# Performance work log

Hardware: AMD Instinct MI355X
Metric: run time of the kernel (lower is better)

## Reference

```python
import jax, jax.numpy as jnp
import numpy as np

NUM_EXPERTS = 8
PHM_DIM = 4


def setup_inputs() -> dict:
    key = jax.random.key(0)
    k1, k2, k3, k4 = jax.random.split(key, 4)
    bsz, seq, D, O, E, p = 4, 2048, 2048, 2048, NUM_EXPERTS, PHM_DIM
    hidden_states = jax.random.normal(k1, (bsz, seq, D), dtype=jnp.float32)
    gate_w = jax.random.normal(k2, (D, E), dtype=jnp.float32) * 0.02
    phm_rule = jax.random.normal(k3, (E, p, p, p), dtype=jnp.float32) * 0.1
    W = jax.random.normal(k4, (E, p, D // p, O // p), dtype=jnp.float32) * 0.02
    b = jnp.zeros((E, O), dtype=jnp.float32)
    return {"hidden_states": hidden_states, "gate_w": gate_w,
            "phm_rule": phm_rule, "W": W, "b": b}


def reference(hidden_states, gate_w, phm_rule, W, b):
    bsz, seq, dim = hidden_states.shape
    E = gate_w.shape[1]
    x = hidden_states.reshape(-1, dim)                      # [T, D]
    logits = x @ gate_w                                     # [T, E]
    prob = jax.nn.softmax(logits, axis=-1)                  # [T, E]
    gate = jnp.argmax(prob, axis=-1)                        # [T]
    # load-balancing loss
    num_tokens = jnp.sum(jax.nn.one_hot(gate, E, dtype=jnp.int32), axis=0)  # [E]
    f = num_tokens.astype(prob.dtype)
    f = f / jnp.sum(f)
    P = jnp.mean(prob, axis=0)
    balance_loss = E * jnp.sum(P * f)
    # PHM weight per expert: H_e = sum_p kron(phm_rule[e,p], W[e,p]) -> [E, D, O]
    Wfull = jnp.einsum('epab,epij->eaibj', phm_rule, W).reshape(E, dim, -1)
    # dense evaluation of every expert on every token, then top-1 select
    all_out = jnp.einsum('td,edo->teo', x, Wfull) + b[None, :, :]  # [T, E, O]
    tok_prob = jnp.take_along_axis(prob, gate[:, None], axis=1)    # [T, 1]
    out = jnp.take_along_axis(all_out, gate[:, None, None], axis=1)[:, 0, :] * tok_prob
    out = out.reshape(bsz, seq, -1)
    return out, balance_loss, num_tokens
```

## Files before the change

### kernel.cpp

```cpp
#include <hip/hip_runtime.h>
#include <cstdint>
#include <cstddef>

typedef _Float16 f16;
typedef f16 f16x2 __attribute__((ext_vector_type(2)));
typedef f16 f16x4 __attribute__((ext_vector_type(4)));
typedef f16 f16x8 __attribute__((ext_vector_type(8)));
typedef float f32x4 __attribute__((ext_vector_type(4)));

#define NEXP 8
#define BM 128
#define BN 128
#define BK 32
#define NSTAGE 3
#define TPW 4

__device__ __forceinline__ void async_cp16(void* lds, const void* gsrc) {
  __builtin_amdgcn_global_load_lds(
      (const __attribute__((address_space(1))) void*)gsrc,
      (__attribute__((address_space(3))) void*)lds, 16, 0, 0);
}

__global__ __launch_bounds__(256) void k_fusedA(
    const float* __restrict__ x, const float* __restrict__ gw,
    f16* __restrict__ xb, int* __restrict__ gate, float* __restrict__ scale,
    int* __restrict__ cnt, float* __restrict__ probsum,
    const float* __restrict__ Wp, const float* __restrict__ rule,
    f16* __restrict__ wt,
    int D, int Dp, int Op, int O, int ngate)
{
  __shared__ __align__(16) uint8_t smem[16960];
  int tid = threadIdx.x;

  if ((int)blockIdx.x < ngate) {
    float (*gws)[516] = (float(*)[516])smem;
    float* ps = (float*)(smem + NEXP * 516 * 4);
    int*   pc = (int*)(smem + NEXP * 516 * 4 + 32);
    int lane = tid & 63, w = tid >> 6;
    if (tid < NEXP) { ps[tid] = 0.f; pc[tid] = 0; }

    int t0 = (blockIdx.x * 4 + w) * TPW;
    const float* xr = x + (size_t)t0 * D;
    f16* xbr = xb + (size_t)t0 * D;

    float acc[TPW][NEXP] = {};
    int nq = D >> 9;
    for (int qp = 0; qp < nq; qp++) {
      __syncthreads();
      const float2* gsrc = (const float2*)(gw + (size_t)qp * 512 * NEXP);
      for (int i = tid; i < 2048; i += 256) {
        float2 v = gsrc[i];
        int f = i * 2;
        int d = f >> 3, e = f & 7;
        gws[e][d] = v.x;
        gws[e + 1][d] = v.y;
      }
      __syncthreads();

      int dh = qp << 9;
#pragma unroll
      for (int it = 0; it < 2; it++) {
        int d0 = lane * 4 + it * 256;
        float4 xv[TPW];
#pragma unroll
        for (int tp = 0; tp < TPW; tp++) {
          xv[tp] = *(const float4*)(xr + (size_t)tp * D + dh + d0);
          f16x4 h;
          h[0] = (f16)xv[tp].x; h[1] = (f16)xv[tp].y;
          h[2] = (f16)xv[tp].z; h[3] = (f16)xv[tp].w;
          *(f16x4*)(xbr + (size_t)tp * D + dh + d0) = h;
        }
#pragma unroll
        for (int e = 0; e < NEXP; e++) {
          float4 g = *(const float4*)&gws[e][d0];
#pragma unroll
          for (int tp = 0; tp < TPW; tp++)
            acc[tp][e] += xv[tp].x * g.x + xv[tp].y * g.y +
                          xv[tp].z * g.z + xv[tp].w * g.w;
        }
      }
    }

#pragma unroll
    for (int tp = 0; tp < TPW; tp++)
#pragma unroll
      for (int e = 0; e < NEXP; e++) {
        float v = acc[tp][e];
        for (int o = 32; o > 0; o >>= 1) v += __shfl_xor(v, o);
        acc[tp][e] = v;
      }

    if (lane == 0) {
#pragma unroll
      for (int tp = 0; tp < TPW; tp++) {
        float m = acc[tp][0]; int g = 0;
#pragma unroll
        for (int e = 1; e < NEXP; e++)
          if (acc[tp][e] > m) { m = acc[tp][e]; g = e; }
        float pr[NEXP]; float ssum = 0.f;
#pragma unroll
        for (int e = 0; e < NEXP; e++) { pr[e] = __expf(acc[tp][e] - m); ssum += pr[e]; }
        float inv = 1.0f / ssum;
#pragma unroll
        for (int e = 0; e < NEXP; e++) atomicAdd(&ps[e], pr[e] * inv);
        atomicAdd(&pc[g], 1);
        gate[t0 + tp] = g;
        scale[t0 + tp] = pr[g] * inv;
      }
    }
    __syncthreads();
    if (tid < NEXP) {
      atomicAdd(&probsum[tid], ps[tid]);
      atomicAdd(&cnt[tid], pc[tid]);
    }
  } else {
    float (*Wt)[32][33] = (float(*)[32][33])smem;
    int bid = blockIdx.x - ngate;
    int it = Dp >> 5, jt = Op >> 5;
    int itile = bid % it; bid /= it;
    int jtile = bid % jt; bid /= jt;
    int e = bid;
    int i0 = itile * 32, j0 = jtile * 32;

    for (int idx = tid; idx < 4096; idx += 256) {
      int p = idx >> 10, rem = idx & 1023, ii = rem >> 5, jj = rem & 31;
      Wt[p][ii][jj] = Wp[(size_t)((e * 4 + p) * Dp + i0 + ii) * Op + j0 + jj];
    }
    __syncthreads();

    int r = tid >> 1;
    int b = r >> 5;
    int jj = r & 31;
    int h = tid & 1;

    float s[4][4];
#pragma unroll
    for (int p = 0; p < 4; p++)
#pragma unroll
      for (int a = 0; a < 4; a++)
        s[p][a] = rule[((e * 4 + p) * 4 + a) * 4 + b];

    f16x8 outv[4][2];
#pragma unroll
    for (int k = 0; k < 16; k++) {
      int i = h * 16 + k;
      float w0 = Wt[0][i][jj], w1 = Wt[1][i][jj];
      float w2 = Wt[2][i][jj], w3 = Wt[3][i][jj];
#pragma unroll
      for (int a = 0; a < 4; a++) {
        float acc = s[0][a] * w0 + s[1][a] * w1 + s[2][a] * w2 + s[3][a] * w3;
        outv[a][k >> 3][k & 7] = (f16)acc;
      }
    }

    size_t rowbase = ((size_t)e * O + (size_t)b * Op + j0 + jj) * D + i0 + h * 16;
#pragma unroll
    for (int a = 0; a < 4; a++) {
      *(f16x8*)(wt + rowbase + (size_t)a * Dp)     = outv[a][0];
      *(f16x8*)(wt + rowbase + (size_t)a * Dp + 8) = outv[a][1];
    }
  }
}

__global__ __launch_bounds__(256) void k_fusedB(
    const int* __restrict__ cnt, const float* __restrict__ probsum,
    const int* __restrict__ gate, int* __restrict__ offs,
    int* __restrict__ ndesc, int2* __restrict__ desc,
    int* __restrict__ cursor, int* __restrict__ perm,
    float* __restrict__ otail, int T)
{
  int tid = threadIdx.x;
  if (blockIdx.x == 0) {
    __shared__ int soffs[NEXP + 1];
    __shared__ int snd;
    __shared__ float sloss;
    __shared__ int2 sdesc[96];
    if (tid == 0) {
      int off = 0, nd = 0; float loss = 0.f;
      for (int e = 0; e < NEXP; e++) {
        soffs[e] = off;
        int c = cnt[e];
        loss += probsum[e] * (float)c;
        for (int m0 = 0; m0 < c; m0 += BM) { sdesc[nd] = make_int2(e, m0); nd++; }
        off += c;
      }
      soffs[NEXP] = off;
      snd = nd;
      sloss = loss;
    }
    __syncthreads();
    if (tid <= NEXP) offs[tid] = soffs[tid];
    if (tid == 9) *ndesc = snd;
    if (tid == 10) {
      float invT = 1.0f / (float)T;
      otail[0] = (float)NEXP * sloss * invT * invT;
    }
    if (tid >= 16 && tid < 16 + NEXP) otail[1 + tid - 16] = (float)cnt[tid - 16];
    for (int i = tid; i < snd; i += 256) desc[i] = sdesc[i];
  } else {
    int t = (blockIdx.x - 1) * 256 + tid;
    int g = gate[t];
    int lane = tid & 63;
    int lofs[NEXP];
    {
      int run = 0;
#pragma unroll
      for (int e = 0; e < NEXP; e++) { lofs[e] = run; run += cnt[e]; }
    }
    int pos = 0;
#pragma unroll
    for (int e = 0; e < NEXP; e++) {
      unsigned long long mask = __ballot(g == e);
      if (mask == 0ull) continue;
      int leader = __ffsll((unsigned long long)mask) - 1;
      int base = 0;
      if (lane == leader) base = atomicAdd(&cursor[e], (int)__popcll(mask));
      base = __shfl(base, leader);
      if (g == e) {
        int below = (int)__popcll(mask & ((1ull << lane) - 1ull));
        pos = lofs[e] + base + below;
      }
    }
    perm[pos] = t;
  }
}

__global__ __launch_bounds__(256) void k_gemm(
    const f16* __restrict__ xb, const f16* __restrict__ wt,
    const float* __restrict__ bias, const int* __restrict__ perm,
    const int* __restrict__ cnt, const int* __restrict__ offs,
    const int* __restrict__ ndesc, const int2* __restrict__ desc,
    const float* __restrict__ scale, float* __restrict__ out, int D, int O)
{
  if ((int)blockIdx.y >= *ndesc) return;
  int2 dsc = desc[blockIdx.y];
  int e = dsc.x, m0 = dsc.y;
  int ce = cnt[e];
  int seg = offs[e];
  int n0 = blockIdx.x * BN;

  __shared__ f16 Al[NSTAGE][BM * BK];
  __shared__ f16 Bl[NSTAGE][BN * BK];
  __shared__ int tokS[BM];
  __shared__ float scS[BM];

  int tid = threadIdx.x;
  if (tid < BM) {
    int idx = m0 + tid; if (idx > ce - 1) idx = ce - 1;
    int tok = perm[seg + idx];
    tokS[tid] = tok;
    scS[tid] = scale[tok];
  }
  __syncthreads();

  int r = tid >> 2;
  int c = tid & 3;
  int gc = c ^ ((r >> 1) & 3);
  const f16* a1 = xb + (size_t)tokS[r] * D + gc * 8;
  const f16* a2 = xb + (size_t)tokS[r + 64] * D + gc * 8;
  const f16* b1 = wt + ((size_t)e * O + n0 + r) * D + gc * 8;
  const f16* b2 = wt + ((size_t)e * O + n0 + r + 64) * D + gc * 8;

  int lane = tid & 63;
  int w = tid >> 6;
  int wm = (w & 1) * 64, wn = (w >> 1) * 64;
  int lr = lane & 15, q = lane >> 4;
  int qs = q ^ ((lr >> 1) & 3);

  f32x4 acc[4][4] = {};
  int nk = D / BK;

#define STAGE(kk, p)                                             \
  do {                                                           \
    async_cp16(&Al[(p)][tid * 8], a1 + (kk) * BK);               \
    async_cp16(&Al[(p)][2048 + tid * 8], a2 + (kk) * BK);        \
    async_cp16(&Bl[(p)][tid * 8], b1 + (kk) * BK);               \
    async_cp16(&Bl[(p)][2048 + tid * 8], b2 + (kk) * BK);        \
  } while (0)

  STAGE(0, 0);
  STAGE(1, 1);
  STAGE(2, 2);

  int p = 0;
  for (int kk = 0; kk < nk; ++kk) {
    int rem = nk - 1 - kk;
    if (rem >= 2)
      asm volatile("s_waitcnt vmcnt(8)\n\ts_barrier" ::: "memory");
    else if (rem == 1)
      asm volatile("s_waitcnt vmcnt(4)\n\ts_barrier" ::: "memory");
    else
      asm volatile("s_waitcnt vmcnt(0)\n\ts_barrier" ::: "memory");

    f16x8 af[4], bf[4];
#pragma unroll
    for (int mi = 0; mi < 4; mi++)
      af[mi] = *(const f16x8*)&Al[p][(wm + mi * 16 + lr) * BK + qs * 8];
#pragma unroll
    for (int ni = 0; ni < 4; ni++)
      bf[ni] = *(const f16x8*)&Bl[p][(wn + ni * 16 + lr) * BK + qs * 8];

    asm volatile("s_waitcnt lgkmcnt(0)\n\ts_barrier" ::: "memory");
    if (kk + NSTAGE < nk) STAGE(kk + NSTAGE, p);

#pragma unroll
    for (int mi = 0; mi < 4; mi++)
#pragma unroll
      for (int ni = 0; ni < 4; ni++)
        acc[mi][ni] = __builtin_amdgcn_mfma_f32_16x16x32_f16(
            af[mi], bf[ni], acc[mi][ni], 0, 0, 0);

    p++; if (p == NSTAGE) p = 0;
  }
#undef STAGE

  float bv[4];
#pragma unroll
  for (int ni = 0; ni < 4; ni++)
    bv[ni] = bias[(size_t)e * O + n0 + wn + ni * 16 + lr];
#pragma unroll
  for (int mi = 0; mi < 4; mi++) {
#pragma unroll
    for (int rg = 0; rg < 4; rg++) {
      int rl = wm + mi * 16 + q * 4 + rg;
      if (m0 + rl < ce) {
        float s = scS[rl];
        float* orow = out + (size_t)tokS[rl] * O + n0 + wn;
#pragma unroll
        for (int ni = 0; ni < 4; ni++)
          orow[ni * 16 + lr] = (acc[mi][ni][rg] + bv[ni]) * s;
      }
    }
  }
}

extern "C" void kernel_launch(void* const* d_in, const int* in_sizes, int n_in,
                              void* d_out, int out_size, void* d_ws, size_t ws_size,
                              hipStream_t stream)
{
  const float* x    = (const float*)d_in[0];
  const float* gw   = (const float*)d_in[1];
  const float* rule = (const float*)d_in[2];
  const float* W    = (const float*)d_in[3];
  const float* bias = (const float*)d_in[4];
  float* out = (float*)d_out;

  int D = in_sizes[1] / NEXP;
  int O = in_sizes[4] / NEXP;
  int T = in_sizes[0] / D;
  int Dp = D / 4, Op = O / 4;

  uint8_t* ws = (uint8_t*)d_ws;
  size_t off = 0;
  f16* xb = (f16*)(ws + off);  off += (size_t)T * D * 2;
  f16* wt = (f16*)(ws + off);  off += (size_t)NEXP * O * D * 2;
  int*   gate  = (int*)(ws + off);   off += (size_t)T * 4;
  float* scale = (float*)(ws + off); off += (size_t)T * 4;
  int*   perm  = (int*)(ws + off);   off += (size_t)T * 4;
  off = (off + 255) & ~(size_t)255;
  uint8_t* C = ws + off;
  int*   cnt     = (int*)(C + 0);
  float* probsum = (float*)(C + 32);
  int*   cursor  = (int*)(C + 64);
  int*   ndesc   = (int*)(C + 96);
  int*   offs    = (int*)(C + 128);
  int2*  desc    = (int2*)(C + 192);

  hipMemsetAsync(C, 0, 128, stream);

  int ngate = T / (4 * TPW);
  int nwf = NEXP * (Op / 32) * (Dp / 32);
  k_fusedA<<<ngate + nwf, 256, 0, stream>>>(
      x, gw, xb, gate, scale, cnt, probsum, W, rule, wt, D, Dp, Op, O, ngate);

  k_fusedB<<<1 + T / 256, 256, 0, stream>>>(
      cnt, probsum, gate, offs, ndesc, desc, cursor, perm,
      out + (size_t)T * O, T);

  int maxdesc = T / BM + NEXP;
  k_gemm<<<dim3(O / BN, maxdesc), 256, 0, stream>>>(
      xb, wt, bias, perm, cnt, offs, ndesc, desc, scale, out, D, O);
}
```

Baseline: 313.6 us.

## Fold routing/permutation kernel into gate kernel via last-block completion counter

Removes the separate k_fusedB launch by having gate blocks write per-block expert probability sums and counts to slots, then the last block to finish (detected by an atomic done counter) reduces them and builds offsets, tile descriptors, the loss and the token permutation. This saves a kernel launch and its dependency gap. The cost is that the permutation over all T tokens is now serialized in one block, and the tail work waits for every gate block.

Result: slower. 376.3 us (+20.0%).

```diff
diff --git a/kernel.cpp b/kernel.cpp
--- a/kernel.cpp
+++ b/kernel.cpp
@@ -24,10 +24,13 @@
 __global__ __launch_bounds__(256) void k_fusedA(
     const float* __restrict__ x, const float* __restrict__ gw,
     f16* __restrict__ xb, int* __restrict__ gate, float* __restrict__ scale,
-    int* __restrict__ cnt, float* __restrict__ probsum,
+    int* __restrict__ cnt, int* __restrict__ done,
+    float* __restrict__ psSlot, int* __restrict__ cntSlot,
+    int* __restrict__ offs, int* __restrict__ ndesc, int2* __restrict__ desc,
+    int* __restrict__ perm, float* __restrict__ otail,
     const float* __restrict__ Wp, const float* __restrict__ rule,
     f16* __restrict__ wt,
-    int D, int Dp, int Op, int O, int ngate)
+    int D, int Dp, int Op, int O, int ngate, int T)
 {
   __shared__ __align__(16) uint8_t smem[16960];
   int tid = threadIdx.x;
@@ -110,8 +113,91 @@
     }
     __syncthreads();
     if (tid < NEXP) {
-      atomicAdd(&probsum[tid], ps[tid]);
-      atomicAdd(&cnt[tid], pc[tid]);
+      psSlot[(size_t)blockIdx.x * NEXP + tid] = ps[tid];
+      cntSlot[blockIdx.x * NEXP + tid] = pc[tid];
+    }
+    __threadfence();
+    __syncthreads();
+    __shared__ int lastFlag;
+    if (tid == 0) {
+      int old = atomicAdd(done, 1);
+      lastFlag = (old == ngate - 1) ? 1 : 0;
+    }
+    __syncthreads();
+    if (!lastFlag) return;
+    __threadfence();
+
+    __shared__ float pps[32][NEXP];
+    __shared__ int   pcs[32][NEXP];
+    __shared__ float rps[NEXP];
+    __shared__ int   rcnt[NEXP];
+    {
+      int e = tid & 7, part = tid >> 3;
+      float s = 0.f; int c = 0;
+      for (int b = part; b < ngate; b += 32) {
+        s += psSlot[(size_t)b * NEXP + e];
+        c += cntSlot[b * NEXP + e];
+      }
+      pps[part][e] = s; pcs[part][e] = c;
+    }
+    __syncthreads();
+    if (tid < NEXP) {
+      float s = 0.f; int c = 0;
+#pragma unroll
+      for (int p2 = 0; p2 < 32; p2++) { s += pps[p2][tid]; c += pcs[p2][tid]; }
+      rps[tid] = s; rcnt[tid] = c;
+      cnt[tid] = c;
+    }
+    __syncthreads();
+
+    __shared__ int soffs[NEXP + 1];
+    __shared__ int snd;
+    __shared__ float sloss;
+    __shared__ int2 sdesc[96];
+    if (tid == 0) {
+      int off = 0, nd = 0; float loss = 0.f;
+      for (int e = 0; e < NEXP; e++) {
+        soffs[e] = off;
+        int c = rcnt[e];
+        loss += rps[e] * (float)c;
+        for (int m0 = 0; m0 < c; m0 += BM) { sdesc[nd] = make_int2(e, m0); nd++; }
+        off += c;
+      }
+      soffs[NEXP] = off;
+      snd = nd;
+      sloss = loss;
+    }
+    __shared__ int lcur[NEXP];
+    if (tid >= 32 && tid < 32 + NEXP) lcur[tid - 32] = 0;
+    __syncthreads();
+    if (tid <= NEXP) offs[tid] = soffs[tid];
+    if (tid == 9) *ndesc = snd;
+    if (tid == 10) {
+      float invT = 1.0f / (float)T;
+      otail[0] = (float)NEXP * sloss * invT * invT;
+    }
+    if (tid >= 16 && tid < 16 + NEXP) otail[1 + tid - 16] = (float)rcnt[tid - 16];
+    for (int i = tid; i < snd; i += 256) desc[i] = sdesc[i];
+
+    int lane2 = tid & 63;
+    for (int base = 0; base < T; base += 256) {
+      int t = base + tid;
+      int g = gate[t];
+      int pos = 0;
+#pragma unroll
+      for (int e = 0; e < NEXP; e++) {
+        unsigned long long mask = __ballot(g == e);
+        if (mask == 0ull) continue;
+        int leader = __ffsll((unsigned long long)mask) - 1;
+        int b2 = 0;
+        if (lane2 == leader) b2 = atomicAdd(&lcur[e], (int)__popcll(mask));
+        b2 = __shfl(b2, leader);
+        if (g == e) {
+          int below = (int)__popcll(mask & ((1ull << lane2) - 1ull));
+          pos = soffs[e] + b2 + below;
+        }
+      }
+      perm[pos] = t;
     }
   } else {
     float (*Wt)[32][33] = (float(*)[32][33])smem;
@@ -159,69 +245,6 @@
       *(f16x8*)(wt + rowbase + (size_t)a * Dp)     = outv[a][0];
       *(f16x8*)(wt + rowbase + (size_t)a * Dp + 8) = outv[a][1];
     }
-  }
-}
-
-__global__ __launch_bounds__(256) void k_fusedB(
-    const int* __restrict__ cnt, const float* __restrict__ probsum,
-    const int* __restrict__ gate, int* __restrict__ offs,
-    int* __restrict__ ndesc, int2* __restrict__ desc,
-    int* __restrict__ cursor, int* __restrict__ perm,
-    float* __restrict__ otail, int T)
-{
-  int tid = threadIdx.x;
-  if (blockIdx.x == 0) {
-    __shared__ int soffs[NEXP + 1];
-    __shared__ int snd;
-    __shared__ float sloss;
-    __shared__ int2 sdesc[96];
-    if (tid == 0) {
-      int off = 0, nd = 0; float loss = 0.f;
-      for (int e = 0; e < NEXP; e++) {
-        soffs[e] = off;
-        int c = cnt[e];
-        loss += probsum[e] * (float)c;
-        for (int m0 = 0; m0 < c; m0 += BM) { sdesc[nd] = make_int2(e, m0); nd++; }
-        off += c;
-      }
-      soffs[NEXP] = off;
-      snd = nd;
-      sloss = loss;
-    }
-    __syncthreads();
-    if (tid <= NEXP) offs[tid] = soffs[tid];
-    if (tid == 9) *ndesc = snd;
-    if (tid == 10) {
-      float invT = 1.0f / (float)T;
-      otail[0] = (float)NEXP * sloss * invT * invT;
-    }
-    if (tid >= 16 && tid < 16 + NEXP) otail[1 + tid - 16] = (float)cnt[tid - 16];
-    for (int i = tid; i < snd; i += 256) desc[i] = sdesc[i];
-  } else {
-    int t = (blockIdx.x - 1) * 256 + tid;
-    int g = gate[t];
-    int lane = tid & 63;
-    int lofs[NEXP];
-    {
-      int run = 0;
-#pragma unroll
-      for (int e = 0; e < NEXP; e++) { lofs[e] = run; run += cnt[e]; }
-    }
-    int pos = 0;
-#pragma unroll
-    for (int e = 0; e < NEXP; e++) {
-      unsigned long long mask = __ballot(g == e);
-      if (mask == 0ull) continue;
-      int leader = __ffsll((unsigned long long)mask) - 1;
-      int base = 0;
-      if (lane == leader) base = atomicAdd(&cursor[e], (int)__popcll(mask));
-      base = __shfl(base, leader);
-      if (g == e) {
-        int below = (int)__popcll(mask & ((1ull << lane) - 1ull));
-        pos = lofs[e] + base + below;
-      }
-    }
-    perm[pos] = t;
   }
 }
 
@@ -360,22 +383,21 @@
   off = (off + 255) & ~(size_t)255;
   uint8_t* C = ws + off;
   int*   cnt     = (int*)(C + 0);
-  float* probsum = (float*)(C + 32);
-  int*   cursor  = (int*)(C + 64);
+  int*   done    = (int*)(C + 64);
   int*   ndesc   = (int*)(C + 96);
   int*   offs    = (int*)(C + 128);
   int2*  desc    = (int2*)(C + 192);
+  float* psSlot  = (float*)(C + 4096);
+  int*   cntSlot = (int*)(C + 4096 + 16384);
 
   hipMemsetAsync(C, 0, 128, stream);
 
   int ngate = T / (4 * TPW);
   int nwf = NEXP * (Op / 32) * (Dp / 32);
   k_fusedA<<<ngate + nwf, 256, 0, stream>>>(
-      x, gw, xb, gate, scale, cnt, probsum, W, rule, wt, D, Dp, Op, O, ngate);
-
-  k_fusedB<<<1 + T / 256, 256, 0, stream>>>(
-      cnt, probsum, gate, offs, ndesc, desc, cursor, perm,
-      out + (size_t)T * O, T);
+      x, gw, xb, gate, scale, cnt, done, psSlot, cntSlot,
+      offs, ndesc, desc, perm, out + (size_t)T * O,
+      W, rule, wt, D, Dp, Op, O, ngate, T);
 
   int maxdesc = T / BM + NEXP;
   k_gemm<<<dim3(O / BN, maxdesc), 256, 0, stream>>>(
```
